# Kernel optimization log

Measured on AMD Instinct MI355X. Metric: run time of the kernel, lower is better.

## Reference

```python
import jax, jax.numpy as jnp
from jax import lax
import numpy as np

K = 9  # nsamples = 3*3 ball-query neighbors
LAYERS = [
    dict(cin=0,    mid=45,   cout=64,   r=1.5, ss=2, tk=1, ts=1, pad=(0, 0)),
    dict(cin=64,   mid=96,   cout=128,  r=3.0, ss=2, tk=3, ts=2, pad=(1, 0)),
    dict(cin=128,  mid=192,  cout=256,  r=3.0, ss=1, tk=3, ts=1, pad=(1, 1)),
    dict(cin=256,  mid=384,  cout=512,  r=6.0, ss=2, tk=3, ts=2, pad=(1, 0)),
    dict(cin=512,  mid=768,  cout=1024, r=6.0, ss=1, tk=3, ts=1, pad=(1, 1)),
    dict(cin=1024, mid=1536, cout=2048, r=6.0, ss=2, tk=1, ts=1, pad=(0, 0)),
]

def furthest_point_sample(xyz, m):
    B, N, _ = xyz.shape
    def step(carry, _):
        mind, last = carry
        lastp = jnp.take_along_axis(xyz, last[:, None, None], axis=1)  # (B,1,3)
        mind = jnp.minimum(mind, jnp.sum((xyz - lastp) ** 2, axis=-1))
        nxt = jnp.argmax(mind, axis=-1).astype(jnp.int32)
        return (mind, nxt), last
    init = (jnp.full((B, N), 1e10, xyz.dtype), jnp.zeros((B,), jnp.int32))
    _, idxs = lax.scan(step, init, None, length=m)
    return jnp.swapaxes(idxs, 0, 1)

def ball_query(radius, k, points, anchors):
    # first-k-within-radius semantics of the pointnet2 CUDA ball_query kernel
    d2 = jnp.sum((anchors[:, :, None, :] - points[:, None, :, :]) ** 2, axis=-1)  # (B,M,N)
    N = points.shape[1]
    mask = d2 < radius * radius
    key = jnp.where(mask, jnp.arange(N, dtype=jnp.int32), N)
    idx = -lax.top_k(-key, k)[0]  # k smallest keys = first k in-radius indices
    first = jnp.argmax(mask, axis=-1).astype(jnp.int32)  # 0 if none in radius (CUDA init)
    return jnp.where(idx < N, idx, first[:, :, None]).astype(jnp.int32)

def pst_conv(xyzs, feats, Wd, Wf, Wt, cfg):
    # xyzs: (B,L,N,3); feats: (B,L,N,Cin) or None (channel-last layout, same math as torch (B,L,C,N))
    B, L, N, _ = xyzs.shape
    p0, p1 = cfg['pad']
    if p0 + p1:
        zx = jnp.zeros((B, 1, N, 3), xyzs.dtype)
        xyzs = jnp.concatenate([zx] * p0 + [xyzs] + [zx] * p1, axis=1)
        if feats is not None:
            zf = jnp.zeros((B, 1, N, feats.shape[-1]), feats.dtype)
            feats = jnp.concatenate([zf] * p0 + [feats] + [zf] * p1, axis=1)
    tr = cfg['tk'] // 2
    m = N // cfg['ss']
    bi = jnp.arange(B)[:, None, None]
    out_x, out_f = [], []
    for t in range(tr, xyzs.shape[1] - tr, cfg['ts']):
        aidx = furthest_point_sample(xyzs[:, t], m)
        anchor = jnp.take_along_axis(xyzs[:, t], aidx[:, :, None], axis=1)  # (B,m,3)
        parts = []
        for i in range(t - tr, t + tr + 1):
            idx = ball_query(cfg['r'], K, xyzs[:, i], anchor)   # (B,m,K)
            nb = xyzs[:, i][bi, idx]                            # (B,m,K,3) gather
            disp = nb - anchor[:, :, None, :]
            d = jnp.einsum('bmkc,oc->bmko', disp, Wd)           # 1x1 conv on displacement
            if feats is not None:
                fg = feats[:, i][bi, idx]                       # (B,m,K,Cin) gather
                sf = jnp.einsum('bmkc,oc->bmko', fg, Wf) * d    # 'multiplication' aggregation
            else:
                sf = d
            parts.append(jnp.sum(sf, axis=2))                   # 'sum' spatial pooling
        nf = jnp.concatenate(parts, axis=-1)                    # (B,m,tk*mid)
        mu = jnp.mean(nf, axis=(0, 1))
        var = jnp.var(nf, axis=(0, 1))
        nf = jax.nn.relu((nf - mu) * lax.rsqrt(var + 1e-5))     # BatchNorm1d (batch stats, affine=identity-init) + ReLU
        nf = jnp.einsum('bmc,oc->bmo', nf, Wt)                  # temporal 1x1 conv
        out_x.append(anchor)
        out_f.append(nf)
    return jnp.stack(out_x, axis=1), jnp.stack(out_f, axis=1)

def _forward(xyzs, Wds, Wfs, Wts, fc_w, fc_b):
    B, S, L, N, C = xyzs.shape
    x = xyzs.reshape(B * S, L, N, C)  # mirrors xyzs.reshape((-1, L_sub_clip, N_point, C_xyz))
    feats = None
    for li, cfg in enumerate(LAYERS):
        x, feats = pst_conv(x, feats, Wds[li], Wfs[li], Wts[li], cfg)
        if li < len(LAYERS) - 1:
            feats = jax.nn.relu(feats)  # F.relu between PSTConv blocks (not after conv4)
    tokens = jnp.einsum('blnc,oc->blno', feats, fc_w) + fc_b  # conv_fc on permuted features
    BT, Lout, M, Cout = tokens.shape  # Lout == 1 per the model's assert
    return tokens.reshape(B, S, M, Cout)

def setup_inputs() -> dict:
    key = jax.random.key(0)
    ks = iter(jax.random.split(key, 40))
    B, S, L, N = 8, 4, 4, 2048
    inp = {'xyzs': jax.random.normal(next(ks), (B, S, L, N, 3), jnp.float32), 'epoch': 1}
    def xav(k, o, i):
        gain = np.sqrt(2.0)  # relu gain, matching get_and_init_FC_layer style init
        bound = gain * np.sqrt(6.0 / (o + i))
        return jax.random.uniform(k, (o, i), jnp.float32, -bound, bound)
    for li, cfg in enumerate(LAYERS):
        inp['d%d' % li] = xav(next(ks), cfg['mid'], 3)
        if cfg['cin']:
            inp['f%d' % li] = xav(next(ks), cfg['mid'], cfg['cin'])
        inp['t%d' % li] = xav(next(ks), cfg['cout'], cfg['tk'] * cfg['mid'])
    inp['fc_w'] = xav(next(ks), 1024, 2048)
    inp['fc_b'] = jnp.zeros((1024,), jnp.float32)
    return inp

def reference(xyzs, d0, d1, d2, d3, d4, d5, f1, f2, f3, f4, f5, t0, t1, t2, t3, t4, t5, fc_w, fc_b, epoch):
    Wds = [d0, d1, d2, d3, d4, d5]
    Wfs = [None, f1, f2, f3, f4, f5]
    Wts = [t0, t1, t2, t3, t4, t5]
    return _forward(xyzs, Wds, Wfs, Wts, fc_w, fc_b)
```

## Files before the change

kernel.cpp:

```cpp
#include <hip/hip_runtime.h>
#include <hip/hip_bf16.h>
#include <math.h>

typedef __hip_bfloat16 bf16;
typedef _Float16 f16;
typedef _Float16 f16x2 __attribute__((ext_vector_type(2)));
typedef _Float16 f16x8 __attribute__((ext_vector_type(8)));
typedef float f32x4 __attribute__((ext_vector_type(4)));

struct Sched { int tt[5]; int fi[5]; int jj[5]; };
struct CvtF32 { const void* src[4]; float* dst[4]; int n[4]; int blk0[5]; };
struct CvtF16 { const void* src[6]; f16* dst[6]; int n[6]; int blk0[7]; };
struct W2J { const void* wd[5]; const void* wf[5]; f16* dst[5]; int mid[5]; int cin[5]; int n[5]; int blk0[6]; };

__global__ void k_detect(const unsigned int* __restrict__ w, int nwords, int* __restrict__ flag,
                         float* __restrict__ zp, int zn){
  if(blockIdx.x==0){
    __shared__ int cnt;
    if(threadIdx.x==0) cnt=0;
    __syncthreads();
    int local=0;
    for(int i=threadIdx.x;i<nwords;i+=256){
      unsigned int v=w[i];
      int e=(v>>7)&0xFF;
      if(e>=0xC0) local++;
    }
    atomicAdd(&cnt, local);
    __syncthreads();
    if(threadIdx.x==0) flag[0] = (cnt > (nwords>>3)) ? 1 : 0;
  } else {
    int i=(blockIdx.x-1)*256+threadIdx.x;
    if(i<zn) zp[i]=0.f;
  }
}

__device__ inline float ldmix(const void* p, size_t i, bool f32m){
  return f32m ? ((const float*)p)[i] : __bfloat162float(((const bf16*)p)[i]);
}

__global__ void k_cvt_all(CvtF32 J, const int* __restrict__ flag){
  int b=blockIdx.x;
  int j=0;
  while(j<3 && J.blk0[j+1]<=b) j++;
  int i=(b-J.blk0[j])*256+threadIdx.x;
  if(i>=J.n[j]) return;
  bool f32m=*flag!=0;
  J.dst[j][i]=ldmix(J.src[j],i,f32m);
}

__global__ void k_cvth_all(CvtF16 J, const int* __restrict__ flag){
  int b=blockIdx.x;
  int j=0;
  while(j<5 && J.blk0[j+1]<=b) j++;
  int i=(b-J.blk0[j])*256+threadIdx.x;
  if(i>=J.n[j]) return;
  bool f32m=*flag!=0;
  J.dst[j][i]=(f16)ldmix(J.src[j],i,f32m);
}

__global__ void k_w2all(W2J J, const int* __restrict__ flag){
  int b=blockIdx.x;
  int j=0;
  while(j<4 && J.blk0[j+1]<=b) j++;
  int i=(b-J.blk0[j])*256+threadIdx.x;
  if(i>=J.n[j]) return;
  int cin=J.cin[j]; int K3=3*cin;
  int o=i/K3; int rem=i-o*K3; int a=rem/cin; int c=rem-a*cin;
  float v=0.f;
  if(o<J.mid[j]){
    bool f32m=*flag!=0;
    v=ldmix(J.wd[j],(size_t)3*o+a,f32m)*ldmix(J.wf[j],(size_t)o*cin+c,f32m);
  }
  J.dst[j][i]=(f16)v;
}

template<int P>
__global__ __launch_bounds__(256) void k_fps2(
    const float* __restrict__ xyz, int L, int N, int m,
    int c0,int c1,int c2,int c3, int T, float* __restrict__ anchors)
{
  __shared__ float4 ptsS[P*256];
  __shared__ unsigned long long keyS[2][4];
  __shared__ float ancS[3*1024];
  int prob=blockIdx.x;
  int b=prob/T, tt=prob%T;
  int f=(tt==0)?c0:(tt==1)?c1:(tt==2)?c2:c3;
  const float* src = xyz + ((size_t)(b*L+f))*N*3;
  float* anc = anchors + ((size_t)(b*T+tt))*m*3;
  int tid=threadIdx.x;
  for(int t=tid;t<N;t+=256)
    ptsS[t]=make_float4(src[3*t],src[3*t+1],src[3*t+2],0.f);
  __syncthreads();
  float px[P],py[P],pz[P],mind[P];
#pragma unroll
  for(int j=0;j<P;j++){
    float4 v=ptsS[tid+j*256];
    px[j]=v.x; py[j]=v.y; pz[j]=v.z; mind[j]=1e10f;
  }
  float4 p0=ptsS[0];
  float lx=p0.x, ly=p0.y, lz=p0.z;
  if(tid==0){ ancS[0]=lx; ancS[1]=ly; ancS[2]=lz; }
  int w=tid>>6;
  for(int it=1; it<m; ++it){
    float bv=-1.f; int bi=0;
#pragma unroll
    for(int j=0;j<P;j++){
#pragma clang fp contract(off)
      float dx=px[j]-lx, dy=py[j]-ly, dz=pz[j]-lz;
      float d2=dx*dx+dy*dy+dz*dz;
      float mv=mind[j]; if(d2<mv) mv=d2; mind[j]=mv;
      if(mv>bv){ bv=mv; bi=tid+j*256; }
    }
    unsigned int hi=__float_as_uint(bv);
    unsigned int lo=0xFFFFFFFFu-(unsigned)bi;
#define DPPSTEP(CTRL) { \
    unsigned int shi=(unsigned)__builtin_amdgcn_update_dpp(0,(int)hi,CTRL,0xF,0xF,true); \
    unsigned int slo=(unsigned)__builtin_amdgcn_update_dpp(0,(int)lo,CTRL,0xF,0xF,true); \
    bool g=(shi>hi)||(shi==hi&&slo>lo); \
    hi=g?shi:hi; lo=g?slo:lo; }
    DPPSTEP(0x111) DPPSTEP(0x112) DPPSTEP(0x114) DPPSTEP(0x118) DPPSTEP(0x142) DPPSTEP(0x143)
#undef DPPSTEP
    if((tid&63)==63)
      keyS[it&1][w]=((unsigned long long)hi<<32)|lo;
    __syncthreads();
    unsigned long long k0=keyS[it&1][0], k1=keyS[it&1][1];
    unsigned long long k2=keyS[it&1][2], k3=keyS[it&1][3];
    unsigned long long ka = k0>k1?k0:k1;
    unsigned long long kb = k2>k3?k2:k3;
    unsigned long long kk = ka>kb?ka:kb;
    int wi = (int)(0xFFFFFFFFu - (unsigned)(kk & 0xFFFFFFFFull));
    float4 wc = ptsS[wi];
    lx=wc.x; ly=wc.y; lz=wc.z;
    if(tid==0){ ancS[3*it]=lx; ancS[3*it+1]=ly; ancS[3*it+2]=lz; }
  }
  __syncthreads();
  for(int t=tid;t<3*m;t+=256) anc[t]=ancS[t];
}

template<int P>
__global__ __launch_bounds__(256) void k_mega(
    const float* __restrict__ xyzF, int Lf, int Nf, int mf,
    int c0,int c1,int c2,int c3, int Tf, float* __restrict__ ancOut, int fpsN,
    int oN, int isP0,
    const f16* __restrict__ featsO, const float* __restrict__ XinO, const float* __restrict__ XoutO,
    const int* __restrict__ bqO, f16* __restrict__ GoN, int mO, int cinO, int NO, int LinO,
    size_t aBSO, int MO, Sched SO, const float* __restrict__ WdO, int midO, int ldO,
    const float* __restrict__ XinB, const float* __restrict__ XoutB, int* __restrict__ bqOut,
    int NB, int mB, float r2B, int LinB, size_t aBSB, int MB, Sched SB, int chunksB)
{
  __shared__ float4 ptsS[P*256];
  __shared__ unsigned long long keyS[2][4];
  __shared__ float sp[768];
  int bid=(int)blockIdx.x;
  if(bid < fpsN){
    int prob=bid;
    int b=prob/Tf, tt=prob%Tf;
    int f=(tt==0)?c0:(tt==1)?c1:(tt==2)?c2:c3;
    const float* src = xyzF + ((size_t)(b*Lf+f))*Nf*3;
    float* anc = ancOut + ((size_t)(b*Tf+tt))*mf*3;
    int tid=threadIdx.x;
    for(int t=tid;t<Nf;t+=256)
      ptsS[t]=make_float4(src[3*t],src[3*t+1],src[3*t+2],0.f);
    __syncthreads();
    float px[P],py[P],pz[P],mind[P];
#pragma unroll
    for(int j=0;j<P;j++){
      float4 v=ptsS[tid+j*256];
      px[j]=v.x; py[j]=v.y; pz[j]=v.z; mind[j]=1e10f;
    }
    float4 p0=ptsS[0];
    float lx=p0.x, ly=p0.y, lz=p0.z;
    if(tid==0){ anc[0]=lx; anc[1]=ly; anc[2]=lz; }
    int w=tid>>6;
    for(int it=1; it<mf; ++it){
      float bv=-1.f; int bi=0;
#pragma unroll
      for(int j=0;j<P;j++){
#pragma clang fp contract(off)
        float dx=px[j]-lx, dy=py[j]-ly, dz=pz[j]-lz;
        float d2=dx*dx+dy*dy+dz*dz;
        float mv=mind[j]; if(d2<mv) mv=d2; mind[j]=mv;
        if(mv>bv){ bv=mv; bi=tid+j*256; }
      }
      unsigned int hi=__float_as_uint(bv);
      unsigned int lo=0xFFFFFFFFu-(unsigned)bi;
#define DPPSTEP(CTRL) { \
      unsigned int shi=(unsigned)__builtin_amdgcn_update_dpp(0,(int)hi,CTRL,0xF,0xF,true); \
      unsigned int slo=(unsigned)__builtin_amdgcn_update_dpp(0,(int)lo,CTRL,0xF,0xF,true); \
      bool g=(shi>hi)||(shi==hi&&slo>lo); \
      hi=g?shi:hi; lo=g?slo:lo; }
      DPPSTEP(0x111) DPPSTEP(0x112) DPPSTEP(0x114) DPPSTEP(0x118) DPPSTEP(0x142) DPPSTEP(0x143)
#undef DPPSTEP
      if((tid&63)==63)
        keyS[it&1][w]=((unsigned long long)hi<<32)|lo;
      __syncthreads();
      unsigned long long k0=keyS[it&1][0], k1=keyS[it&1][1];
      unsigned long long k2=keyS[it&1][2], k3=keyS[it&1][3];
      unsigned long long ka = k0>k1?k0:k1;
      unsigned long long kb = k2>k3?k2:k3;
      unsigned long long kk = ka>kb?ka:kb;
      int wi = (int)(0xFFFFFFFFu - (unsigned)(kk & 0xFFFFFFFFull));
      float4 wc = ptsS[wi];
      lx=wc.x; ly=wc.y; lz=wc.z;
      if(tid==0){ anc[3*it]=lx; anc[3*it+1]=ly; anc[3*it+2]=lz; }
    }
  } else if(bid < fpsN + oN){
    int ob = bid - fpsN;
    if(isP0){
      int quarter = MO>>2;
      int tt = ob / quarter, rb = ob - tt*quarter;
      int sub = threadIdx.x>>6;
      int o = threadIdx.x&63;
      int row = rb*4 + sub;
      int b = row/mO, mm = row - b*mO;
      const float* A = XoutO + (size_t)b*aBSO + (size_t)tt*mO*3 + (size_t)mm*3;
      float ax=A[0], ay=A[1], az=A[2];
      float w0=0,w1=0,w2=0;
      if(o<midO){ w0=WdO[3*o]; w1=WdO[3*o+1]; w2=WdO[3*o+2]; }
      int fr=SO.fi[tt];
      int nmask=NO-1;
      const int* id = bqO + ((size_t)tt*MO + row)*9;
      const float* Pb = XinO + ((size_t)b*LinO+fr)*(size_t)NO*3;
      float acc=0.f;
      for(int k=0;k<9;k++){
        int p=id[k] & nmask;
        const float* q = Pb + (size_t)p*3;
        float dx=q[0]-ax, dy=q[1]-ay, dz=q[2]-az;
        acc += dx*w0+dy*w1+dz*w2;
      }
      if(o<midO) GoN[(size_t)tt*MO*ldO + (size_t)row*ldO + o] = (f16)acc;
    } else {
      int cw2 = cinO>>1; if(cw2>256) cw2=256;
      int rpb = 256/cw2;
      int tid=threadIdx.x;
      int sub=tid/cw2, lc=tid-sub*cw2;
      int r=ob*rpb+sub;
      int Kp=3*cinO;
      int nmask=NO-1;
      int s=r/MO, mrow=r-s*MO;
      int b=mrow/mO, mm=mrow-b*mO;
      int tt=SO.tt[s], fr=SO.fi[s];
      const float* A0=XoutO+(size_t)b*aBSO+(size_t)tt*mO*3+(size_t)mm*3;
      float ax=A0[0],ay=A0[1],az=A0[2];
      const float* Pb=XinO+((size_t)b*LinO+fr)*(size_t)NO*3;
      const f16* Fb=featsO+(((size_t)b*LinO+fr)*(size_t)NO)*(size_t)cinO;
      const int* id=bqO+(size_t)r*9;
      int idx[9]; float d0[9],d1[9],d2a[9];
#pragma unroll
      for(int k=0;k<9;k++){
        int p=id[k]&nmask; idx[k]=p;
        const float* q=Pb+(size_t)p*3;
        d0[k]=q[0]-ax; d1[k]=q[1]-ay; d2a[k]=q[2]-az;
      }
      f16* Gr=GoN+(size_t)r*Kp;
      for(int cc=2*lc; cc<cinO; cc+=2*cw2){
        float a0=0,a1=0,a2=0,b0=0,b1=0,b2=0;
#pragma unroll
        for(int k=0;k<9;k++){
          f16x2 fv=*(const f16x2*)(Fb+(size_t)idx[k]*cinO+cc);
          float f0=(float)fv[0], f1=(float)fv[1];
          a0=fmaf(d0[k],f0,a0); b0=fmaf(d0[k],f1,b0);
          a1=fmaf(d1[k],f0,a1); b1=fmaf(d1[k],f1,b1);
          a2=fmaf(d2a[k],f0,a2); b2=fmaf(d2a[k],f1,b2);
        }
        f16x2 o0={(f16)a0,(f16)b0}, o1={(f16)a1,(f16)b1}, o2={(f16)a2,(f16)b2};
        *(f16x2*)(Gr+cc)=o0; *(f16x2*)(Gr+cinO+cc)=o1; *(f16x2*)(Gr+2*cinO+cc)=o2;
      }
    }
  } else {
    int fb=bid-fpsN-oN;
    int s=fb/(32*chunksB);
    int rem=fb-s*(32*chunksB);
    int b=rem/chunksB;
    int a=(rem-b*chunksB)*256+threadIdx.x;
    int tt=SB.tt[s], fr=SB.fi[s];
    const float* Pb = XinB + ((size_t)b*LinB + fr)*(size_t)NB*3;
    bool act = a<mB;
    float ax=0,ay=0,az=0;
    int* o = bqOut + ((size_t)s*MB + (size_t)b*mB + (size_t)(act?a:0))*9;
    if(act){
      const float* A=XoutB+(size_t)b*aBSB+(size_t)tt*mB*3+(size_t)a*3;
      ax=A[0]; ay=A[1]; az=A[2];
    }
    int cnt = act?0:9, first=0;
    for(int base=0; base<NB; base+=256){
      for(int t=threadIdx.x; t<768; t+=256) sp[t]=Pb[(size_t)base*3+t];
      __syncthreads();
      for(int q=0;q<256;q++){
#pragma clang fp contract(off)
        float dx=sp[3*q]-ax, dy=sp[3*q+1]-ay, dz=sp[3*q+2]-az;
        float d2=dx*dx+dy*dy+dz*dz;
        if(d2<r2B && cnt<9){
          int p=base+q;
          if(cnt==0) first=p;
          o[cnt]=p; cnt++;
        }
      }
      if(__syncthreads_and(cnt>=9)) break;
    }
    if(act){ for(int k=cnt;k<9;k++) o[k]=first; }
  }
}

__global__ __launch_bounds__(256) void k_outer(
    const f16* __restrict__ feats, const float* __restrict__ Xin,
    const float* __restrict__ Xout, const int* __restrict__ bqAll,
    f16* __restrict__ Gh, int m, int cin, int N, int Lin,
    size_t aBS, int nmask, int M, Sched S)
{
  int cw2 = cin>>1; if(cw2>256) cw2=256;
  int rpb = 256/cw2;
  int tid=threadIdx.x;
  int sub=tid/cw2, lc=tid-sub*cw2;
  int r=blockIdx.x*rpb+sub;
  int Kp=3*cin;
  int s=r/M, mrow=r-s*M;
  int b=mrow/m, mm=mrow-b*m;
  int tt=S.tt[s], fr=S.fi[s];
  const float* A0=Xout+(size_t)b*aBS+(size_t)tt*m*3+(size_t)mm*3;
  float ax=A0[0],ay=A0[1],az=A0[2];
  const float* Pb=Xin+((size_t)b*Lin+fr)*(size_t)N*3;
  const f16* Fb=feats+(((size_t)b*Lin+fr)*(size_t)N)*(size_t)cin;
  const int* id=bqAll+(size_t)r*9;
  int idx[9]; float d0[9],d1[9],d2a[9];
#pragma unroll
  for(int k=0;k<9;k++){
    int p=id[k]&nmask; idx[k]=p;
    const float* q=Pb+(size_t)p*3;
    d0[k]=q[0]-ax; d1[k]=q[1]-ay; d2a[k]=q[2]-az;
  }
  f16* Gr=Gh+(size_t)r*Kp;
  for(int cc=2*lc; cc<cin; cc+=2*cw2){
    float a0=0,a1=0,a2=0,b0=0,b1=0,b2=0;
#pragma unroll
    for(int k=0;k<9;k++){
      f16x2 fv=*(const f16x2*)(Fb+(size_t)idx[k]*cin+cc);
      float f0=(float)fv[0], f1=(float)fv[1];
      a0=fmaf(d0[k],f0,a0); b0=fmaf(d0[k],f1,b0);
      a1=fmaf(d1[k],f0,a1); b1=fmaf(d1[k],f1,b1);
      a2=fmaf(d2a[k],f0,a2); b2=fmaf(d2a[k],f1,b2);
    }
    f16x2 o0={(f16)a0,(f16)b0}, o1={(f16)a1,(f16)b1}, o2={(f16)a2,(f16)b2};
    *(f16x2*)(Gr+cc)=o0; *(f16x2*)(Gr+cin+cc)=o1; *(f16x2*)(Gr+2*cin+cc)=o2;
  }
}

__global__ __launch_bounds__(256) void k_pg(
    const f16* __restrict__ Gh, const f16* __restrict__ W2,
    f16* __restrict__ nfh, int Kp, int mid, int C, int M, Sched S)
{
  __shared__ f16 As[128*40];
  __shared__ f16 Bs[128*40];
  int tid=threadIdx.x;
  int lane=tid&63, w=tid>>6;
  int quad=lane>>4, l15=lane&15;
  int rowOff=(w>>1)*64, colOff=(w&1)*64;
  int rowBase=blockIdx.x*128, colBase=blockIdx.y*128;
  f32x4 acc[4][4];
#pragma unroll
  for(int i=0;i<4;i++)
#pragma unroll
    for(int j=0;j<4;j++) acc[i][j]=(f32x4){0.f,0.f,0.f,0.f};
  int nct=Kp>>5;
  int srow=tid>>1, shalf=tid&1;
  for(int ct=0;ct<nct;ct++){
    __syncthreads();
    {
      const uint4* s=(const uint4*)(Gh+(size_t)(rowBase+srow)*Kp+(ct<<5)+(shalf<<4));
      uint4 u0=s[0], u1=s[1];
      *(uint4*)(As + srow*40 + (shalf<<4))     = u0;
      *(uint4*)(As + srow*40 + (shalf<<4) + 8) = u1;
    }
    {
      const uint4* s=(const uint4*)(W2+(size_t)(colBase+srow)*Kp+(ct<<5)+(shalf<<4));
      uint4 u0=s[0], u1=s[1];
      *(uint4*)(Bs + srow*40 + (shalf<<4))     = u0;
      *(uint4*)(Bs + srow*40 + (shalf<<4) + 8) = u1;
    }
    __syncthreads();
    f16x8 af[4], bf4[4];
#pragma unroll
    for(int rt=0;rt<4;rt++) af[rt]=*(const f16x8*)(As + (rowOff+rt*16+l15)*40 + quad*8);
#pragma unroll
    for(int ctl=0;ctl<4;ctl++) bf4[ctl]=*(const f16x8*)(Bs + (colOff+ctl*16+l15)*40 + quad*8);
#pragma unroll
    for(int rt=0;rt<4;rt++)
#pragma unroll
      for(int ctl=0;ctl<4;ctl++)
        acc[rt][ctl]=__builtin_amdgcn_mfma_f32_16x16x32_f16(af[rt],bf4[ctl],acc[rt][ctl],0,0,0);
  }
#pragma unroll
  for(int rt=0;rt<4;rt++){
#pragma unroll
    for(int r=0;r<4;r++){
      int row=rowBase+rowOff+rt*16+quad*4+r;
      int s=row/M, mrow=row-s*M;
      int tt=S.tt[s], j=S.jj[s];
      f16* base = nfh + (size_t)tt*M*C + (size_t)mrow*C + j*mid;
#pragma unroll
      for(int ctl=0;ctl<4;ctl++){
        int col=colBase+colOff+ctl*16+l15;
        if(col<mid) base[col]=(f16)acc[rt][ctl][r];
      }
    }
  }
}

__global__ void k_bnstat(const f16* __restrict__ nfh, int M, int C, float* __restrict__ sumsL,
                         int mid, int4 jm, int sumStride){
  int c = blockIdx.x*256 + threadIdx.x;
  if(c>=C) return;
  int tt=blockIdx.z;
  int jmask = (tt==0)?jm.x:(tt==1)?jm.y:(tt==2)?jm.z:jm.w;
  int j=c/mid;
  if(!((jmask>>j)&1)) return;
  const f16* base=nfh+(size_t)tt*M*C;
  int rows = M>>5;
  int r0 = blockIdx.y*rows, r1 = r0+rows;
  float s=0.f, s2=0.f;
  for(int r=r0;r<r1;r++){
    float v=(float)base[(size_t)r*C+c];
    s+=v; s2+=v*v;
  }
  atomicAdd(&sumsL[tt*sumStride+c], s);
  atomicAdd(&sumsL[tt*sumStride+C+c], s2);
}

__global__ void k_bnfin(const float* __restrict__ sumsL, float* __restrict__ scbAll,
                        int C, int M, int mid, int4 jm, int sumStride, int scbStride){
  int c = blockIdx.x*256 + threadIdx.x;
  if(c>=C) return;
  int tt=blockIdx.y;
  int jmask = (tt==0)?jm.x:(tt==1)?jm.y:(tt==2)?jm.z:jm.w;
  float* scb=scbAll+(size_t)tt*scbStride;
  int j=c/mid;
  if(!((jmask>>j)&1)){ scb[c]=0.f; scb[C+c]=0.f; return; }
  float mean=sumsL[tt*sumStride+c]/(float)M;
  float var=sumsL[tt*sumStride+C+c]/(float)M - mean*mean;
  if(var<0.f) var=0.f;
  float rs=1.0f/sqrtf(var+1e-5f);
  scb[c]=rs; scb[C+c]=-mean*rs;
}

template<bool RELU, bool DYN, bool BNA>
__global__ __launch_bounds__(256) void k_gemm_mfma(
    const f16* __restrict__ Ag, const f16* __restrict__ Bh,
    const float* __restrict__ bias, void* __restrict__ out,
    int K, int N, int mloc, size_t oBS, size_t ttA, size_t ttO,
    const int* __restrict__ oflag, const float* __restrict__ scbAll, int scbStride)
{
  __shared__ f16 As[128*40];
  __shared__ f16 Bs[128*40];
  int tid=threadIdx.x;
  int lane=tid&63, w=tid>>6;
  int quad=lane>>4, l15=lane&15;
  int rowOff=(w>>1)*64, colOff=(w&1)*64;
  int rowBase=blockIdx.x*128, colBase=blockIdx.y*128;
  int tt=blockIdx.z;
  const f16* A0=Ag+(size_t)tt*ttA;
  const float* scb = BNA ? (scbAll+(size_t)tt*scbStride) : nullptr;
  f32x4 acc[4][4];
#pragma unroll
  for(int i=0;i<4;i++)
#pragma unroll
    for(int j=0;j<4;j++) acc[i][j]=(f32x4){0.f,0.f,0.f,0.f};
  int nct=K>>5;
  int srow=tid>>1, shalf=tid&1;
  for(int ct=0;ct<nct;ct++){
    __syncthreads();
    {
      int c0g=(ct<<5)+(shalf<<4);
      const f16* src=A0+(size_t)(rowBase+srow)*K+c0g;
      if(BNA){
        f16x8 x0=((const f16x8*)src)[0], x1=((const f16x8*)src)[1];
        f16x8 h0,h1;
#pragma unroll
        for(int q=0;q<8;q++){
          h0[q]=(f16)fmaxf(fmaf((float)x0[q],scb[c0g+q],scb[K+c0g+q]),0.f);
          h1[q]=(f16)fmaxf(fmaf((float)x1[q],scb[c0g+8+q],scb[K+c0g+8+q]),0.f);
        }
        *(f16x8*)(As+srow*40+(shalf<<4))=h0;
        *(f16x8*)(As+srow*40+(shalf<<4)+8)=h1;
      } else {
        const uint4* s=(const uint4*)src;
        uint4 u0=s[0],u1=s[1];
        *(uint4*)(As+srow*40+(shalf<<4))=u0;
        *(uint4*)(As+srow*40+(shalf<<4)+8)=u1;
      }
    }
    {
      const uint4* s=(const uint4*)(Bh+(size_t)(colBase+srow)*K+(ct<<5)+(shalf<<4));
      uint4 u0=s[0], u1=s[1];
      *(uint4*)(Bs + srow*40 + (shalf<<4))     = u0;
      *(uint4*)(Bs + srow*40 + (shalf<<4) + 8) = u1;
    }
    __syncthreads();
    f16x8 af[4], bf4[4];
#pragma unroll
    for(int rt=0;rt<4;rt++) af[rt]=*(const f16x8*)(As + (rowOff+rt*16+l15)*40 + quad*8);
#pragma unroll
    for(int ctl=0;ctl<4;ctl++) bf4[ctl]=*(const f16x8*)(Bs + (colOff+ctl*16+l15)*40 + quad*8);
#pragma unroll
    for(int rt=0;rt<4;rt++)
#pragma unroll
      for(int ctl=0;ctl<4;ctl++)
        acc[rt][ctl]=__builtin_amdgcn_mfma_f32_16x16x32_f16(af[rt],bf4[ctl],acc[rt][ctl],0,0,0);
  }
  bool f32m = DYN ? (*oflag!=0) : true;
#pragma unroll
  for(int rt=0;rt<4;rt++){
#pragma unroll
    for(int r=0;r<4;r++){
      int row=rowBase+rowOff+rt*16+quad*4+r;
      int rb=row/mloc, rm=row-rb*mloc;
      size_t obase=(size_t)rb*oBS + (size_t)tt*ttO + (size_t)rm*N;
#pragma unroll
      for(int ctl=0;ctl<4;ctl++){
        int col=colBase+colOff+ctl*16+l15;
        float v=acc[rt][ctl][r];
        if(bias) v+=bias[col];
        if(RELU) v=fmaxf(v,0.f);
        if(DYN){
          if(!f32m) ((bf16*)out)[obase+col]=__float2bfloat16(v);
          else      ((float*)out)[obase+col]=v;
        } else {
          ((f16*)out)[obase+col]=(f16)v;
        }
      }
    }
  }
}

__global__ __launch_bounds__(256) void k_gemm0(
    const f16* __restrict__ nfh, const float* __restrict__ Wg,
    f16* __restrict__ out, int M, int K, int N, int mloc, size_t oBS, size_t ttO,
    const float* __restrict__ scbAll, int scbStride)
{
  __shared__ alignas(16) float As[16][64];
  __shared__ alignas(16) float Bs[16][64];
  int tid=threadIdx.x, tx=tid&15, ty=tid>>4;
  int rowBase=blockIdx.x*64, colBase=blockIdx.y*64;
  int tt=blockIdx.z;
  const f16* A0=nfh+(size_t)tt*M*K;
  const float* scb=scbAll+(size_t)tt*scbStride;
  float acc[4][4];
#pragma unroll
  for(int i=0;i<4;i++)
#pragma unroll
    for(int j=0;j<4;j++) acc[i][j]=0.f;
  int lrow=tid&63, lcq=tid>>6;
  int nct=(K+15)>>4;
  for(int ct=0;ct<nct;ct++){
    __syncthreads();
    {
      int r=rowBase+lrow, c0=(ct<<4)+(lcq<<2);
#pragma unroll
      for(int q=0;q<4;q++){
        int c=c0+q;
        As[(lcq<<2)+q][lrow] = (c<K)? fmaxf(fmaf((float)A0[(size_t)r*K+c],scb[c],scb[K+c]),0.f) : 0.f;
      }
    }
    {
      int og=colBase+lrow, c0=(ct<<4)+(lcq<<2);
#pragma unroll
      for(int q=0;q<4;q++){
        int c=c0+q;
        Bs[(lcq<<2)+q][lrow] = (c<K)? Wg[(size_t)og*K+c] : 0.f;
      }
    }
    __syncthreads();
#pragma unroll
    for(int c=0;c<16;c++){
      float4 a4=*(const float4*)&As[c][ty<<2];
      float av[4]={a4.x,a4.y,a4.z,a4.w};
      float4 b4=*(const float4*)&Bs[c][tx<<2];
      float bw[4]={b4.x,b4.y,b4.z,b4.w};
#pragma unroll
      for(int i=0;i<4;i++)
#pragma unroll
        for(int j=0;j<4;j++) acc[i][j]+=av[i]*bw[j];
    }
  }
#pragma unroll
  for(int i=0;i<4;i++){
    int r=rowBase+(ty<<2)+i;
    int rb=r/mloc, rm=r-rb*mloc;
    size_t obase=(size_t)rb*oBS + (size_t)blockIdx.z*ttO + (size_t)rm*N;
#pragma unroll
    for(int j=0;j<4;j++){
      int o=colBase+(tx<<2)+j;
      out[obase+o]=(f16)fmaxf(acc[i][j],0.f);
    }
  }
}

extern "C" void kernel_launch(void* const* d_in, const int* in_sizes, int n_in,
                              void* d_out, int out_size, void* d_ws, size_t ws_size,
                              hipStream_t stream) {
  (void)in_sizes; (void)n_in; (void)out_size; (void)ws_size;

  const int di[6] = {2,4,7,10,13,16};
  const int fi6[6] = {-1,5,8,11,14,17};
  const int ti[6] = {3,6,9,12,15,18};

  const int midv[6]={45,96,192,384,768,1536};
  const int midp[6]={0,128,256,384,768,1536};
  const int cinv[6]={0,64,128,256,512,1024};
  const int coutv[6]={64,128,256,512,1024,2048};
  const int tkv[6]={1,3,3,3,3,1};
  const int Nv[6]={2048,1024,512,512,256,256};
  const int mv[6]={1024,512,512,256,256,128};
  const int Lv[6]={4,4,2,2,1,1};
  const int Tv[6]={4,2,2,1,1,1};
  const float rrv[6]={1.5f,3.f,3.f,6.f,6.f,6.f};

  float* ws=(float*)d_ws;
  size_t off=0;
  auto A=[&](size_t n)->float*{ float* p=ws+off; off+=(n+63)&~(size_t)63; return p; };
  auto Ah=[&](size_t n)->f16*{ return (f16*)A((n+1)/2); };

  int* flag=(int*)A(64);

  f16* W2h[6]; W2h[0]=nullptr;
  for(int l=1;l<6;l++) W2h[l]=Ah((size_t)midp[l]*3*cinv[l]);
  f16* Wth[6]; Wth[0]=nullptr;
  for(int l=1;l<6;l++) Wth[l]=Ah((size_t)coutv[l]*tkv[l]*midv[l]);
  float* Wd0=A(135);
  float* Wt0=A(2880);
  f16* fcwh=Ah(2097152);
  float* fcb=A(1024);

  float* X[7];
  X[0]=A(786432);
  for(int l=0;l<6;l++) X[l+1]=A((size_t)32*Tv[l]*mv[l]*3);

  f16* FA=Ah(8388608);
  f16* FB=Ah(8388608);
  f16* F[7]; F[0]=nullptr;
  for(int l=0;l<6;l++) F[l+1]=(l%2==0)?FA:FB;

  f16* nfh=Ah(18874368);
  float* sumsAll=A(11*4608);
  float* scbAll=A(4*4608);
  f16* Gh=Ah(25165824);
  int* bqA=(int*)A(1179648);
  int* bqB=(int*)A(1179648);
  int* bqBuf[2]={bqA,bqB};

  {
    int zn=11*4608;
    int zb=(zn+255)/256;
    k_detect<<<dim3(1+zb),dim3(256),0,stream>>>((const unsigned int*)d_in[0], 4096, flag, sumsAll, zn);
  }
  {
    CvtF32 J;
    J.src[0]=d_in[0];  J.dst[0]=X[0];  J.n[0]=786432;
    J.src[1]=d_in[3];  J.dst[1]=Wt0;   J.n[1]=2880;
    J.src[2]=d_in[20]; J.dst[2]=fcb;   J.n[2]=1024;
    J.src[3]=d_in[2];  J.dst[3]=Wd0;   J.n[3]=135;
    J.blk0[0]=0; J.blk0[1]=3072; J.blk0[2]=3084; J.blk0[3]=3088; J.blk0[4]=3089;
    k_cvt_all<<<dim3(3089),dim3(256),0,stream>>>(J,flag);
  }
  {
    CvtF16 J;
    int ns[6]={36864,147456,589824,2359296,3145728,2097152};
    const void* ss[6]={d_in[ti[1]],d_in[ti[2]],d_in[ti[3]],d_in[ti[4]],d_in[ti[5]],d_in[19]};
    f16* ds[6]={Wth[1],Wth[2],Wth[3],Wth[4],Wth[5],fcwh};
    int bp=0;
    for(int j2=0;j2<6;j2++){ J.src[j2]=ss[j2]; J.dst[j2]=ds[j2]; J.n[j2]=ns[j2]; J.blk0[j2]=bp; bp+=(ns[j2]+255)/256; }
    J.blk0[6]=bp;
    k_cvth_all<<<dim3((unsigned)bp),dim3(256),0,stream>>>(J,flag);
  }
  {
    W2J J;
    int bp=0;
    for(int l=1;l<6;l++){
      int j2=l-1;
      J.wd[j2]=d_in[di[l]]; J.wf[j2]=d_in[fi6[l]]; J.dst[j2]=W2h[l];
      J.mid[j2]=midv[l]; J.cin[j2]=cinv[l]; J.n[j2]=midp[l]*3*cinv[l];
      J.blk0[j2]=bp; bp+=(J.n[j2]+255)/256;
    }
    J.blk0[5]=bp;
    k_w2all<<<dim3((unsigned)bp),dim3(256),0,stream>>>(J,flag);
  }

  const int SLOTS[6]={4,5,4,2,1,1};
  const int sTT[6][5]={{0,1,2,3,0},{0,0,1,1,1},{0,0,1,1,0},{0,0,0,0,0},{0,0,0,0,0},{0,0,0,0,0}};
  const int sFI[6][5]={{0,1,2,3,0},{0,1,1,2,3},{0,1,0,1,0},{0,1,0,0,0},{0,0,0,0,0},{0,0,0,0,0}};
  const int sJJ[6][5]={{0,0,0,0,0},{1,2,0,1,2},{1,2,0,1,0},{1,2,0,0,0},{1,0,0,0,0},{0,0,0,0,0}};
  const int4 jm4[6]={{1,1,1,1},{6,7,0,0},{6,3,0,0},{6,0,0,0},{2,0,0,0},{1,0,0,0}};
  const int Tcenters[6][4]={{0,1,2,3},{0,2,0,0},{0,1,0,0},{0,0,0,0},{0,0,0,0},{0,0,0,0}};
  const int slotBase[6]={0,4,6,8,9,10};

  Sched Sl[6];
  for(int l=0;l<6;l++)
    for(int s=0;s<5;s++){ Sl[l].tt[s]=sTT[l][s]; Sl[l].fi[s]=sFI[l][s]; Sl[l].jj[s]=sJJ[l][s]; }

  auto bqGeo=[&](int lb, int& bqN, int& chunks){
    chunks=(mv[lb]+255)>>8;
    bqN=SLOTS[lb]*32*chunks;
  };

  k_fps2<8><<<dim3(128),dim3(256),0,stream>>>(X[0],4,2048,1024,0,1,2,3,4,X[1]);

  {
    int bqN,chunks; bqGeo(0,bqN,chunks);
    int fpsN=32*Tv[1];
    k_mega<4><<<dim3((unsigned)(fpsN+bqN)),dim3(256),0,stream>>>(
        X[1],Lv[1],Nv[1],mv[1],Tcenters[1][0],Tcenters[1][1],Tcenters[1][2],Tcenters[1][3],Tv[1],X[2],fpsN,
        0,0, FA,X[0],X[1],bqA,nfh,mv[0],1,Nv[0],Lv[0],(size_t)Tv[0]*mv[0]*3,32*mv[0],Sl[0],Wd0,1,1,
        X[0],X[1],bqBuf[0],Nv[0],mv[0],rrv[0]*rrv[0],Lv[0],(size_t)Tv[0]*mv[0]*3,32*mv[0],Sl[0],chunks);
  }

  for(int l=0;l<6;l++){
    int N=Nv[l], m=mv[l], Lin=Lv[l], T=Tv[l], cin=cinv[l], mid=midv[l];
    int C=tkv[l]*midv[l], M=32*m, cout=coutv[l];
    size_t aBS=(size_t)T*m*3;

    if(l<5){
      int lb=l+1;
      int bqN,chunksB; bqGeo(lb,bqN,chunksB);
      size_t aBSB=(size_t)Tv[lb]*mv[lb]*3;
      int MB=32*mv[lb];
      int oN, isP0;
      if(l==0){ isP0=1; oN=M; }
      else{
        isP0=0;
        int cw2=cin>>1; if(cw2>256) cw2=256;
        int rpb=256/cw2;
        oN=SLOTS[l]*M/rpb;
      }
      const f16* featsO=(l==0)?FA:F[l];
      f16* GoN=(l==0)?nfh:Gh;
      int fpsN=0, lf=l+2;
      if(lf<=5) fpsN=32*Tv[lf];
      int a0=0,a1=0,a2=0,a3=0;
      if(lf<=5){ a0=Tcenters[lf][0]; a1=Tcenters[lf][1]; a2=Tcenters[lf][2]; a3=Tcenters[lf][3]; }
      const float* xyzF=(lf<=5)?X[lf]:X[5];
      float* ancOut=(lf<=5)?X[lf+1]:X[6];
      int Lf=(lf<=5)?Lv[lf]:1, Nf=(lf<=5)?Nv[lf]:256, mf=(lf<=5)?mv[lf]:1, Tf=(lf<=5)?Tv[lf]:1;
      dim3 g((unsigned)(fpsN+oN+bqN)), blk(256);
      if(lf<=5 && Nv[lf]==512)
        k_mega<2><<<g,blk,0,stream>>>(xyzF,Lf,Nf,mf,a0,a1,a2,a3,Tf,ancOut,fpsN,
            oN,isP0, featsO,X[l],X[l+1],bqBuf[l&1],GoN,m,cin,N,Lin,aBS,M,Sl[l],Wd0,mid,C,
            X[lb],X[lb+1],bqBuf[lb&1],Nv[lb],mv[lb],rrv[lb]*rrv[lb],Lv[lb],aBSB,MB,Sl[lb],chunksB);
      else
        k_mega<1><<<g,blk,0,stream>>>(xyzF,Lf,Nf,mf,a0,a1,a2,a3,Tf,ancOut,fpsN,
            oN,isP0, featsO,X[l],X[l+1],bqBuf[l&1],GoN,m,cin,N,Lin,aBS,M,Sl[l],Wd0,mid,C,
            X[lb],X[lb+1],bqBuf[lb&1],Nv[lb],mv[lb],rrv[lb]*rrv[lb],Lv[lb],aBSB,MB,Sl[lb],chunksB);
    } else {
      int cw2=cin>>1; if(cw2>256) cw2=256;
      int rpb=256/cw2;
      k_outer<<<dim3((unsigned)(SLOTS[l]*M/rpb)),256,0,stream>>>(
          F[l],X[l],X[l+1],bqBuf[l&1],Gh,m,cin,N,Lin,aBS,N-1,M,Sl[l]);
    }

    if(l>=1)
      k_pg<<<dim3((unsigned)(SLOTS[l]*M/128),(unsigned)(midp[l]/128)),256,0,stream>>>(
          Gh,W2h[l],nfh,3*cin,mid,C,M,Sl[l]);

    float* sumsL=sumsAll+(size_t)slotBase[l]*4608;
    k_bnstat<<<dim3((C+255)/256,32,T),256,0,stream>>>(nfh,M,C,sumsL,mid,jm4[l],4608);
    k_bnfin<<<dim3((C+255)/256,T),256,0,stream>>>(sumsL,scbAll,C,M,mid,jm4[l],4608,4608);

    size_t oBS=(size_t)T*m*cout;
    size_t ttO=(size_t)m*cout;
    if(l==0)
      k_gemm0<<<dim3(M/64,1,4),256,0,stream>>>(nfh,Wt0,F[1],M,C,cout,m,oBS,ttO,scbAll,4608);
    else if(l<5)
      k_gemm_mfma<true,false,true><<<dim3(M/128,cout/128,T),256,0,stream>>>(
          nfh,Wth[l],nullptr,F[l+1],C,cout,m,oBS,(size_t)M*C,ttO,nullptr,scbAll,4608);
    else
      k_gemm_mfma<false,false,true><<<dim3(M/128,cout/128,T),256,0,stream>>>(
          nfh,Wth[l],nullptr,F[l+1],C,cout,m,oBS,(size_t)M*C,ttO,nullptr,scbAll,4608);
  }

  k_gemm_mfma<false,true,false><<<dim3(4096/128,1024/128,1),256,0,stream>>>(
      F[6],fcwh,fcb,d_out,2048,1024,128,(size_t)128*1024,0,0,flag,nullptr,0);
}
```

Baseline: 2.683 ms.

## Fuse BN statistics into pg GEMM epilogue and BN finalize into consumer GEMMs

Moves the per-channel sum and sum-of-squares accumulation into the k_pg MFMA epilogue using shuffles and atomics, which removes the separate k_bnstat pass over nfh for layers 1-5. The k_bnfin kernel is dropped; each consumer GEMM block now recomputes scale and bias from the raw sums into shared memory. The weight-conversion kernels are merged into the first FPS launch as extra blocks, so conversion runs alongside the long FPS. In exchange the design adds atomic contention, redundant finalize work in every GEMM block, and a zero-sum test in place of the old jmask logic for unused channels.

```diff
diff --git a/kernel.cpp b/kernel.cpp
--- a/kernel.cpp
+++ b/kernel.cpp
@@ -48,93 +48,92 @@
   J.dst[j][i]=ldmix(J.src[j],i,f32m);
 }
 
-__global__ void k_cvth_all(CvtF16 J, const int* __restrict__ flag){
-  int b=blockIdx.x;
-  int j=0;
-  while(j<5 && J.blk0[j+1]<=b) j++;
-  int i=(b-J.blk0[j])*256+threadIdx.x;
-  if(i>=J.n[j]) return;
-  bool f32m=*flag!=0;
-  J.dst[j][i]=(f16)ldmix(J.src[j],i,f32m);
-}
-
-__global__ void k_w2all(W2J J, const int* __restrict__ flag){
-  int b=blockIdx.x;
-  int j=0;
-  while(j<4 && J.blk0[j+1]<=b) j++;
-  int i=(b-J.blk0[j])*256+threadIdx.x;
-  if(i>=J.n[j]) return;
-  int cin=J.cin[j]; int K3=3*cin;
-  int o=i/K3; int rem=i-o*K3; int a=rem/cin; int c=rem-a*cin;
-  float v=0.f;
-  if(o<J.mid[j]){
-    bool f32m=*flag!=0;
-    v=ldmix(J.wd[j],(size_t)3*o+a,f32m)*ldmix(J.wf[j],(size_t)o*cin+c,f32m);
-  }
-  J.dst[j][i]=(f16)v;
-}
-
-template<int P>
-__global__ __launch_bounds__(256) void k_fps2(
-    const float* __restrict__ xyz, int L, int N, int m,
-    int c0,int c1,int c2,int c3, int T, float* __restrict__ anchors)
+__global__ __launch_bounds__(256) void k_fps0m(
+    const float* __restrict__ xyz, float* __restrict__ anchors,
+    CvtF16 J16, W2J JW, const int* __restrict__ flag, int cvtB)
 {
-  __shared__ float4 ptsS[P*256];
+  __shared__ float4 ptsS[8*256];
   __shared__ unsigned long long keyS[2][4];
   __shared__ float ancS[3*1024];
-  int prob=blockIdx.x;
-  int b=prob/T, tt=prob%T;
-  int f=(tt==0)?c0:(tt==1)?c1:(tt==2)?c2:c3;
-  const float* src = xyz + ((size_t)(b*L+f))*N*3;
-  float* anc = anchors + ((size_t)(b*T+tt))*m*3;
-  int tid=threadIdx.x;
-  for(int t=tid;t<N;t+=256)
-    ptsS[t]=make_float4(src[3*t],src[3*t+1],src[3*t+2],0.f);
-  __syncthreads();
-  float px[P],py[P],pz[P],mind[P];
-#pragma unroll
-  for(int j=0;j<P;j++){
-    float4 v=ptsS[tid+j*256];
-    px[j]=v.x; py[j]=v.y; pz[j]=v.z; mind[j]=1e10f;
-  }
-  float4 p0=ptsS[0];
-  float lx=p0.x, ly=p0.y, lz=p0.z;
-  if(tid==0){ ancS[0]=lx; ancS[1]=ly; ancS[2]=lz; }
-  int w=tid>>6;
-  for(int it=1; it<m; ++it){
-    float bv=-1.f; int bi=0;
-#pragma unroll
-    for(int j=0;j<P;j++){
+  int bid=(int)blockIdx.x;
+  if(bid<128){
+    const int L=4, N=2048, m=1024, T=4;
+    int prob=bid;
+    int b=prob/T, tt=prob%T;
+    int f=tt;
+    const float* src = xyz + ((size_t)(b*L+f))*N*3;
+    float* anc = anchors + ((size_t)(b*T+tt))*m*3;
+    int tid=threadIdx.x;
+    for(int t=tid;t<N;t+=256)
+      ptsS[t]=make_float4(src[3*t],src[3*t+1],src[3*t+2],0.f);
+    __syncthreads();
+    float px[8],py[8],pz[8],mind[8];
+#pragma unroll
+    for(int j=0;j<8;j++){
+      float4 v=ptsS[tid+j*256];
+      px[j]=v.x; py[j]=v.y; pz[j]=v.z; mind[j]=1e10f;
+    }
+    float4 p0=ptsS[0];
+    float lx=p0.x, ly=p0.y, lz=p0.z;
+    if(tid==0){ ancS[0]=lx; ancS[1]=ly; ancS[2]=lz; }
+    int w=tid>>6;
+    for(int it=1; it<m; ++it){
+      float bv=-1.f; int bi=0;
+#pragma unroll
+      for(int j=0;j<8;j++){
 #pragma clang fp contract(off)
-      float dx=px[j]-lx, dy=py[j]-ly, dz=pz[j]-lz;
-      float d2=dx*dx+dy*dy+dz*dz;
-      float mv=mind[j]; if(d2<mv) mv=d2; mind[j]=mv;
-      if(mv>bv){ bv=mv; bi=tid+j*256; }
-    }
-    unsigned int hi=__float_as_uint(bv);
-    unsigned int lo=0xFFFFFFFFu-(unsigned)bi;
+        float dx=px[j]-lx, dy=py[j]-ly, dz=pz[j]-lz;
+        float d2=dx*dx+dy*dy+dz*dz;
+        float mv=mind[j]; if(d2<mv) mv=d2; mind[j]=mv;
+        if(mv>bv){ bv=mv; bi=tid+j*256; }
+      }
+      unsigned int hi=__float_as_uint(bv);
+      unsigned int lo=0xFFFFFFFFu-(unsigned)bi;
 #define DPPSTEP(CTRL) { \
-    unsigned int shi=(unsigned)__builtin_amdgcn_update_dpp(0,(int)hi,CTRL,0xF,0xF,true); \
-    unsigned int slo=(unsigned)__builtin_amdgcn_update_dpp(0,(int)lo,CTRL,0xF,0xF,true); \
-    bool g=(shi>hi)||(shi==hi&&slo>lo); \
-    hi=g?shi:hi; lo=g?slo:lo; }
-    DPPSTEP(0x111) DPPSTEP(0x112) DPPSTEP(0x114) DPPSTEP(0x118) DPPSTEP(0x142) DPPSTEP(0x143)
+      unsigned int shi=(unsigned)__builtin_amdgcn_update_dpp(0,(int)hi,CTRL,0xF,0xF,true); \
+      unsigned int slo=(unsigned)__builtin_amdgcn_update_dpp(0,(int)lo,CTRL,0xF,0xF,true); \
+      bool g=(shi>hi)||(shi==hi&&slo>lo); \
+      hi=g?shi:hi; lo=g?slo:lo; }
+      DPPSTEP(0x111) DPPSTEP(0x112) DPPSTEP(0x114) DPPSTEP(0x118) DPPSTEP(0x142) DPPSTEP(0x143)
 #undef DPPSTEP
-    if((tid&63)==63)
-      keyS[it&1][w]=((unsigned long long)hi<<32)|lo;
-    __syncthreads();
-    unsigned long long k0=keyS[it&1][0], k1=keyS[it&1][1];
-    unsigned long long k2=keyS[it&1][2], k3=keyS[it&1][3];
-    unsigned long long ka = k0>k1?k0:k1;
-    unsigned long long kb = k2>k3?k2:k3;
-    unsigned long long kk = ka>kb?ka:kb;
-    int wi = (int)(0xFFFFFFFFu - (unsigned)(kk & 0xFFFFFFFFull));
-    float4 wc = ptsS[wi];
-    lx=wc.x; ly=wc.y; lz=wc.z;
-    if(tid==0){ ancS[3*it]=lx; ancS[3*it+1]=ly; ancS[3*it+2]=lz; }
-  }
-  __syncthreads();
-  for(int t=tid;t<3*m;t+=256) anc[t]=ancS[t];
+      if((tid&63)==63)
+        keyS[it&1][w]=((unsigned long long)hi<<32)|lo;
+      __syncthreads();
+      unsigned long long k0=keyS[it&1][0], k1=keyS[it&1][1];
+      unsigned long long k2=keyS[it&1][2], k3=keyS[it&1][3];
+      unsigned long long ka = k0>k1?k0:k1;
+      unsigned long long kb = k2>k3?k2:k3;
+      unsigned long long kk = ka>kb?ka:kb;
+      int wi = (int)(0xFFFFFFFFu - (unsigned)(kk & 0xFFFFFFFFull));
+      float4 wc = ptsS[wi];
+      lx=wc.x; ly=wc.y; lz=wc.z;
+      if(tid==0){ ancS[3*it]=lx; ancS[3*it+1]=ly; ancS[3*it+2]=lz; }
+    }
+    __syncthreads();
+    for(int t=tid;t<3*m;t+=256) anc[t]=ancS[t];
+  } else if(bid < 128+cvtB){
+    int b=bid-128;
+    int j=0;
+    while(j<5 && J16.blk0[j+1]<=b) j++;
+    int i=(b-J16.blk0[j])*256+threadIdx.x;
+    if(i>=J16.n[j]) return;
+    bool f32m=*flag!=0;
+    J16.dst[j][i]=(f16)ldmix(J16.src[j],i,f32m);
+  } else {
+    int b=bid-128-cvtB;
+    int j=0;
+    while(j<4 && JW.blk0[j+1]<=b) j++;
+    int i=(b-JW.blk0[j])*256+threadIdx.x;
+    if(i>=JW.n[j]) return;
+    int cin=JW.cin[j]; int K3=3*cin;
+    int o=i/K3; int rem=i-o*K3; int a=rem/cin; int c=rem-a*cin;
+    float v=0.f;
+    if(o<JW.mid[j]){
+      bool f32m=*flag!=0;
+      v=ldmix(JW.wd[j],(size_t)3*o+a,f32m)*ldmix(JW.wf[j],(size_t)o*cin+c,f32m);
+    }
+    JW.dst[j][i]=(f16)v;
+  }
 }
 
 template<int P>
@@ -347,7 +346,8 @@
 
 __global__ __launch_bounds__(256) void k_pg(
     const f16* __restrict__ Gh, const f16* __restrict__ W2,
-    f16* __restrict__ nfh, int Kp, int mid, int C, int M, Sched S)
+    f16* __restrict__ nfh, int Kp, int mid, int C, int M, Sched S,
+    float* __restrict__ sumsL, int sumStride)
 {
   __shared__ f16 As[128*40];
   __shared__ f16 Bs[128*40];
@@ -388,6 +388,26 @@
 #pragma unroll
       for(int ctl=0;ctl<4;ctl++)
         acc[rt][ctl]=__builtin_amdgcn_mfma_f32_16x16x32_f16(af[rt],bf4[ctl],acc[rt][ctl],0,0,0);
+  }
+  int s0=rowBase/M;
+  int tt0=S.tt[s0], j0=S.jj[s0];
+#pragma unroll
+  for(int ctl=0;ctl<4;ctl++){
+    int gcol=colBase+colOff+ctl*16+l15;
+    float cs=0.f, cq=0.f;
+#pragma unroll
+    for(int rt=0;rt<4;rt++)
+#pragma unroll
+      for(int r=0;r<4;r++){
+        float v=(float)(f16)acc[rt][ctl][r];
+        cs+=v; cq+=v*v;
+      }
+    cs+=__shfl_xor(cs,16); cq+=__shfl_xor(cq,16);
+    cs+=__shfl_xor(cs,32); cq+=__shfl_xor(cq,32);
+    if(quad==0 && gcol<mid){
+      atomicAdd(&sumsL[tt0*sumStride + j0*mid + gcol], cs);
+      atomicAdd(&sumsL[tt0*sumStride + C + j0*mid + gcol], cq);
+    }
   }
 #pragma unroll
   for(int rt=0;rt<4;rt++){
@@ -426,31 +446,16 @@
   atomicAdd(&sumsL[tt*sumStride+C+c], s2);
 }
 
-__global__ void k_bnfin(const float* __restrict__ sumsL, float* __restrict__ scbAll,
-                        int C, int M, int mid, int4 jm, int sumStride, int scbStride){
-  int c = blockIdx.x*256 + threadIdx.x;
-  if(c>=C) return;
-  int tt=blockIdx.y;
-  int jmask = (tt==0)?jm.x:(tt==1)?jm.y:(tt==2)?jm.z:jm.w;
-  float* scb=scbAll+(size_t)tt*scbStride;
-  int j=c/mid;
-  if(!((jmask>>j)&1)){ scb[c]=0.f; scb[C+c]=0.f; return; }
-  float mean=sumsL[tt*sumStride+c]/(float)M;
-  float var=sumsL[tt*sumStride+C+c]/(float)M - mean*mean;
-  if(var<0.f) var=0.f;
-  float rs=1.0f/sqrtf(var+1e-5f);
-  scb[c]=rs; scb[C+c]=-mean*rs;
-}
-
 template<bool RELU, bool DYN, bool BNA>
 __global__ __launch_bounds__(256) void k_gemm_mfma(
     const f16* __restrict__ Ag, const f16* __restrict__ Bh,
     const float* __restrict__ bias, void* __restrict__ out,
     int K, int N, int mloc, size_t oBS, size_t ttA, size_t ttO,
-    const int* __restrict__ oflag, const float* __restrict__ scbAll, int scbStride)
+    const int* __restrict__ oflag, const float* __restrict__ sumsAll, int sumStride, float invM)
 {
   __shared__ f16 As[128*40];
   __shared__ f16 Bs[128*40];
+  __shared__ float scbL[BNA?2*2304:2];
   int tid=threadIdx.x;
   int lane=tid&63, w=tid>>6;
   int quad=lane>>4, l15=lane&15;
@@ -458,7 +463,16 @@
   int rowBase=blockIdx.x*128, colBase=blockIdx.y*128;
   int tt=blockIdx.z;
   const f16* A0=Ag+(size_t)tt*ttA;
-  const float* scb = BNA ? (scbAll+(size_t)tt*scbStride) : nullptr;
+  if(BNA){
+    const float* sm=sumsAll+(size_t)tt*sumStride;
+    for(int c=tid;c<K;c+=256){
+      float s1=sm[c], s2=sm[K+c];
+      float mean=s1*invM;
+      float var=s2*invM-mean*mean; if(var<0.f) var=0.f;
+      float rs=(s2==0.f)?0.f:(1.0f/sqrtf(var+1e-5f));
+      scbL[c]=rs; scbL[K+c]=-mean*rs;
+    }
+  }
   f32x4 acc[4][4];
 #pragma unroll
   for(int i=0;i<4;i++)
@@ -476,8 +490,8 @@
         f16x8 h0,h1;
 #pragma unroll
         for(int q=0;q<8;q++){
-          h0[q]=(f16)fmaxf(fmaf((float)x0[q],scb[c0g+q],scb[K+c0g+q]),0.f);
-          h1[q]=(f16)fmaxf(fmaf((float)x1[q],scb[c0g+8+q],scb[K+c0g+8+q]),0.f);
+          h0[q]=(f16)fmaxf(fmaf((float)x0[q],scbL[c0g+q],scbL[K+c0g+q]),0.f);
+          h1[q]=(f16)fmaxf(fmaf((float)x1[q],scbL[c0g+8+q],scbL[K+c0g+8+q]),0.f);
         }
         *(f16x8*)(As+srow*40+(shalf<<4))=h0;
         *(f16x8*)(As+srow*40+(shalf<<4)+8)=h1;
@@ -534,15 +548,25 @@
 __global__ __launch_bounds__(256) void k_gemm0(
     const f16* __restrict__ nfh, const float* __restrict__ Wg,
     f16* __restrict__ out, int M, int K, int N, int mloc, size_t oBS, size_t ttO,
-    const float* __restrict__ scbAll, int scbStride)
+    const float* __restrict__ sumsAll, int sumStride, float invM)
 {
   __shared__ alignas(16) float As[16][64];
   __shared__ alignas(16) float Bs[16][64];
+  __shared__ float scbL[128];
   int tid=threadIdx.x, tx=tid&15, ty=tid>>4;
   int rowBase=blockIdx.x*64, colBase=blockIdx.y*64;
   int tt=blockIdx.z;
   const f16* A0=nfh+(size_t)tt*M*K;
-  const float* scb=scbAll+(size_t)tt*scbStride;
+  {
+    const float* sm=sumsAll+(size_t)tt*sumStride;
+    for(int c=tid;c<K;c+=256){
+      float s1=sm[c], s2=sm[K+c];
+      float mean=s1*invM;
+      float var=s2*invM-mean*mean; if(var<0.f) var=0.f;
+      float rs=(s2==0.f)?0.f:(1.0f/sqrtf(var+1e-5f));
+      scbL[c]=rs; scbL[K+c]=-mean*rs;
+    }
+  }
   float acc[4][4];
 #pragma unroll
   for(int i=0;i<4;i++)
@@ -557,7 +581,7 @@
 #pragma unroll
       for(int q=0;q<4;q++){
         int c=c0+q;
-        As[(lcq<<2)+q][lrow] = (c<K)? fmaxf(fmaf((float)A0[(size_t)r*K+c],scb[c],scb[K+c]),0.f) : 0.f;
+        As[(lcq<<2)+q][lrow] = (c<K)? fmaxf(fmaf((float)A0[(size_t)r*K+c],scbL[c],scbL[K+c]),0.f) : 0.f;
       }
     }
     {
@@ -641,7 +665,6 @@
 
   f16* nfh=Ah(18874368);
   float* sumsAll=A(11*4608);
-  float* scbAll=A(4*4608);
   f16* Gh=Ah(25165824);
   int* bqA=(int*)A(1179648);
   int* bqB=(int*)A(1179648);
@@ -661,34 +684,31 @@
     J.blk0[0]=0; J.blk0[1]=3072; J.blk0[2]=3084; J.blk0[3]=3088; J.blk0[4]=3089;
     k_cvt_all<<<dim3(3089),dim3(256),0,stream>>>(J,flag);
   }
+
+  CvtF16 J16; int bp16=0;
   {
-    CvtF16 J;
     int ns[6]={36864,147456,589824,2359296,3145728,2097152};
     const void* ss[6]={d_in[ti[1]],d_in[ti[2]],d_in[ti[3]],d_in[ti[4]],d_in[ti[5]],d_in[19]};
     f16* ds[6]={Wth[1],Wth[2],Wth[3],Wth[4],Wth[5],fcwh};
-    int bp=0;
-    for(int j2=0;j2<6;j2++){ J.src[j2]=ss[j2]; J.dst[j2]=ds[j2]; J.n[j2]=ns[j2]; J.blk0[j2]=bp; bp+=(ns[j2]+255)/256; }
-    J.blk0[6]=bp;
-    k_cvth_all<<<dim3((unsigned)bp),dim3(256),0,stream>>>(J,flag);
-  }
+    for(int j2=0;j2<6;j2++){ J16.src[j2]=ss[j2]; J16.dst[j2]=ds[j2]; J16.n[j2]=ns[j2]; J16.blk0[j2]=bp16; bp16+=(ns[j2]+255)/256; }
+    J16.blk0[6]=bp16;
+  }
+  W2J JW; int bpw2=0;
   {
-    W2J J;
-    int bp=0;
     for(int l=1;l<6;l++){
       int j2=l-1;
-      J.wd[j2]=d_in[di[l]]; J.wf[j2]=d_in[fi6[l]]; J.dst[j2]=W2h[l];
-      J.mid[j2]=midv[l]; J.cin[j2]=cinv[l]; J.n[j2]=midp[l]*3*cinv[l];
-      J.blk0[j2]=bp; bp+=(J.n[j2]+255)/256;
-    }
-    J.blk0[5]=bp;
-    k_w2all<<<dim3((unsigned)bp),dim3(256),0,stream>>>(J,flag);
+      JW.wd[j2]=d_in[di[l]]; JW.wf[j2]=d_in[fi6[l]]; JW.dst[j2]=W2h[l];
+      JW.mid[j2]=midv[l]; JW.cin[j2]=cinv[l]; JW.n[j2]=midp[l]*3*cinv[l];
+      JW.blk0[j2]=bpw2; bpw2+=(JW.n[j2]+255)/256;
+    }
+    JW.blk0[5]=bpw2;
   }
 
   const int SLOTS[6]={4,5,4,2,1,1};
   const int sTT[6][5]={{0,1,2,3,0},{0,0,1,1,1},{0,0,1,1,0},{0,0,0,0,0},{0,0,0,0,0},{0,0,0,0,0}};
   const int sFI[6][5]={{0,1,2,3,0},{0,1,1,2,3},{0,1,0,1,0},{0,1,0,0,0},{0,0,0,0,0},{0,0,0,0,0}};
   const int sJJ[6][5]={{0,0,0,0,0},{1,2,0,1,2},{1,2,0,1,0},{1,2,0,0,0},{1,0,0,0,0},{0,0,0,0,0}};
-  const int4 jm4[6]={{1,1,1,1},{6,7,0,0},{6,3,0,0},{6,0,0,0},{2,0,0,0},{1,0,0,0}};
+  const int4 jm4l0={1,1,1,1};
   const int Tcenters[6][4]={{0,1,2,3},{0,2,0,0},{0,1,0,0},{0,0,0,0},{0,0,0,0},{0,0,0,0}};
   const int slotBase[6]={0,4,6,8,9,10};
 
@@ -701,7 +721,7 @@
     bqN=SLOTS[lb]*32*chunks;
   };
 
-  k_fps2<8><<<dim3(128),dim3(256),0,stream>>>(X[0],4,2048,1024,0,1,2,3,4,X[1]);
+  k_fps0m<<<dim3((unsigned)(128+bp16+bpw2)),dim3(256),0,stream>>>(X[0],X[1],J16,JW,flag,bp16);
 
   {
     int bqN,chunks; bqGeo(0,bqN,chunks);
@@ -716,6 +736,7 @@
     int N=Nv[l], m=mv[l], Lin=Lv[l], T=Tv[l], cin=cinv[l], mid=midv[l];
     int C=tkv[l]*midv[l], M=32*m, cout=coutv[l];
     size_t aBS=(size_t)T*m*3;
+    float* sumsL=sumsAll+(size_t)slotBase[l]*4608;
 
     if(l<5){
       int lb=l+1;
@@ -757,24 +778,23 @@
 
     if(l>=1)
       k_pg<<<dim3((unsigned)(SLOTS[l]*M/128),(unsigned)(midp[l]/128)),256,0,stream>>>(
-          Gh,W2h[l],nfh,3*cin,mid,C,M,Sl[l]);
-
-    float* sumsL=sumsAll+(size_t)slotBase[l]*4608;
-    k_bnstat<<<dim3((C+255)/256,32,T),256,0,stream>>>(nfh,M,C,sumsL,mid,jm4[l],4608);
-    k_bnfin<<<dim3((C+255)/256,T),256,0,stream>>>(sumsL,scbAll,C,M,mid,jm4[l],4608,4608);
+          Gh,W2h[l],nfh,3*cin,mid,C,M,Sl[l],sumsL,4608);
+    else
+      k_bnstat<<<dim3((C+255)/256,32,T),256,0,stream>>>(nfh,M,C,sumsL,mid,jm4l0,4608);
 
     size_t oBS=(size_t)T*m*cout;
     size_t ttO=(size_t)m*cout;
+    float invM=1.0f/(float)M;
     if(l==0)
-      k_gemm0<<<dim3(M/64,1,4),256,0,stream>>>(nfh,Wt0,F[1],M,C,cout,m,oBS,ttO,scbAll,4608);
+      k_gemm0<<<dim3(M/64,1,4),256,0,stream>>>(nfh,Wt0,F[1],M,C,cout,m,oBS,ttO,sumsL,4608,invM);
     else if(l<5)
       k_gemm_mfma<true,false,true><<<dim3(M/128,cout/128,T),256,0,stream>>>(
-          nfh,Wth[l],nullptr,F[l+1],C,cout,m,oBS,(size_t)M*C,ttO,nullptr,scbAll,4608);
+          nfh,Wth[l],nullptr,F[l+1],C,cout,m,oBS,(size_t)M*C,ttO,nullptr,sumsL,4608,invM);
     else
       k_gemm_mfma<false,false,true><<<dim3(M/128,cout/128,T),256,0,stream>>>(
-          nfh,Wth[l],nullptr,F[l+1],C,cout,m,oBS,(size_t)M*C,ttO,nullptr,scbAll,4608);
+          nfh,Wth[l],nullptr,F[l+1],C,cout,m,oBS,(size_t)M*C,ttO,nullptr,sumsL,4608,invM);
   }
 
   k_gemm_mfma<false,true,false><<<dim3(4096/128,1024/128,1),256,0,stream>>>(
-      F[6],fcwh,fcb,d_out,2048,1024,128,(size_t)128*1024,0,0,flag,nullptr,0);
-}
+      F[6],fcwh,fcb,d_out,2048,1024,128,(size_t)128*1024,0,0,flag,nullptr,0,0.f);
+}
```

Measured after the change: 2.191 ms. -18.3%, faster.
